# Kernel optimization log

Hardware: AMD Instinct MI355X
Metric: run time of the kernel (lower is better)

The kernel has to match this reference:

```python
import jax, jax.numpy as jnp
import numpy as np

N = 50000
IN_F = 256
HID = 32
HEADS = 4
NEG_SLOPE = 0.2


def _gat_layer(x, edge_index, W, a_src, a_dst, bias):
    # x: [N, Fin]; W: [Fin, H*C]; a_src/a_dst: [H, C]; bias: [H*C]
    n = x.shape[0]
    H, C = a_src.shape
    h = (x @ W).reshape(n, H, C)                     # [N, H, C]
    alpha_src = jnp.einsum('nhc,hc->nh', h, a_src)   # [N, H]
    alpha_dst = jnp.einsum('nhc,hc->nh', h, a_dst)   # [N, H]
    src, dst = edge_index[0], edge_index[1]
    logits = alpha_src[src] + alpha_dst[dst]         # [E, H]
    logits = jax.nn.leaky_relu(logits, negative_slope=NEG_SLOPE)
    # segment softmax over edges grouped by destination node
    seg_max = jax.ops.segment_max(logits, dst, num_segments=n)
    seg_max = jnp.where(jnp.isfinite(seg_max), seg_max, 0.0)
    e = jnp.exp(logits - seg_max[dst])               # [E, H]
    denom = jax.ops.segment_sum(e, dst, num_segments=n)  # [N, H]
    attn = e / (denom[dst] + 1e-16)                  # [E, H]
    msg = h[src] * attn[:, :, None]                  # [E, H, C]
    out = jax.ops.segment_sum(msg, dst, num_segments=n)  # [N, H, C]
    return out.reshape(n, H * C) + bias


def _add_self_loops(edge_index, n):
    # PyG GATConv default add_self_loops=True
    loops = jnp.arange(n, dtype=edge_index.dtype)
    return jnp.concatenate([edge_index, jnp.stack([loops, loops])], axis=1)


def setup_inputs() -> dict:
    key = jax.random.key(0)
    ks = jax.random.split(key, 10)
    x = jax.random.normal(ks[0], (N, IN_F), dtype=jnp.float32)
    edge_index = jax.random.randint(ks[1], (2, 800000), 0, N, dtype=jnp.int64)
    d1 = HEADS * HID
    s1 = 1.0 / np.sqrt(IN_F)
    W1 = jax.random.normal(ks[2], (IN_F, d1), dtype=jnp.float32) * s1
    a_src1 = jax.random.normal(ks[3], (HEADS, HID), dtype=jnp.float32) * 0.1
    a_dst1 = jax.random.normal(ks[4], (HEADS, HID), dtype=jnp.float32) * 0.1
    b1 = jnp.zeros((d1,), dtype=jnp.float32)
    s2 = 1.0 / np.sqrt(d1)
    W2 = jax.random.normal(ks[5], (d1, d1), dtype=jnp.float32) * s2
    a_src2 = jax.random.normal(ks[6], (HEADS, HID), dtype=jnp.float32) * 0.1
    a_dst2 = jax.random.normal(ks[7], (HEADS, HID), dtype=jnp.float32) * 0.1
    b2 = jnp.zeros((d1,), dtype=jnp.float32)
    return {"x": x, "edge_index": edge_index, "W1": W1, "a_src1": a_src1,
            "a_dst1": a_dst1, "b1": b1, "W2": W2, "a_src2": a_src2,
            "a_dst2": a_dst2, "b2": b2}


def reference(x, edge_index, W1, a_src1, a_dst1, b1, W2, a_src2, a_dst2, b2):
    # Inference mode: dropout layers are identity.
    ei = _add_self_loops(edge_index, x.shape[0])
    h = _gat_layer(x, ei, W1, a_src1, a_dst1, b1)
    h = jax.nn.elu(h)
    h = _gat_layer(h, ei, W2, a_src2, a_dst2, b2)
    return h
```

## Files before the change

### kernel.cpp

```cpp
#include <hip/hip_runtime.h>
#include <hip/hip_fp16.h>
#include <math.h>

#define HEADS 4
#define HID 32
#define D1 128
#define IN_FEAT 256
#define NEG_SLOPE 0.2f
#define CAP 64
#define AGG_NODES 4
#define NPASS 8
#define EPT 8

#define WTS_STRIDE_H 72
#define HTS_STRIDE_H 136
#define SMEM_BYTES (128 * 272)

typedef _Float16 half8 __attribute__((ext_vector_type(8)));
typedef float f32x4 __attribute__((ext_vector_type(4)));
typedef long long ll2 __attribute__((ext_vector_type(2)));

static inline int ceil_div(int a, int b) { return (a + b - 1) / b; }

static __device__ inline float2 unpack_h2(unsigned int v) {
    __half2 h = __builtin_bit_cast(__half2, v);
    return __half22float2(h);
}

static __device__ inline void fma_mix_lo(float& a, unsigned int h2, float w) {
    asm("v_fma_mix_f32 %0, %1, %2, %0 op_sel:[0,0,0] op_sel_hi:[1,0,0]"
        : "+v"(a) : "v"(h2), "v"(w));
}
static __device__ inline void fma_mix_hi(float& a, unsigned int h2, float w) {
    asm("v_fma_mix_f32 %0, %1, %2, %0 op_sel:[1,0,0] op_sel_hi:[1,0,0]"
        : "+v"(a) : "v"(h2), "v"(w));
}

__global__ void init_prep(const unsigned int* __restrict__ raw, int* __restrict__ flag,
                          const float* __restrict__ W1, _Float16* __restrict__ WT1,
                          const float* __restrict__ W2, _Float16* __restrict__ WT2) {
    int i = blockIdx.x * blockDim.x + threadIdx.x;
    if (i < IN_FEAT * D1) {
        int k = i >> 7, n = i & 127;
        WT1[(size_t)n * IN_FEAT + k] = (_Float16)W1[i];
    }
    if (i < D1 * D1) {
        int k = i >> 7, n = i & 127;
        WT2[(size_t)n * D1 + k] = (_Float16)W2[i];
    }
    if (blockIdx.x == 0 && threadIdx.x < 64) {
        unsigned int hi = raw[2 * threadIdx.x + 1];
        unsigned long long b = __ballot(hi != 0u);
        if (threadIdx.x == 0) *flag = (b == 0ULL) ? 1 : 0;
    }
}

__device__ void scatter_body(int sbid, const void* __restrict__ raw,
                             const int* __restrict__ flag,
                             int* __restrict__ cnt,
                             unsigned short* __restrict__ slots,
                             int E, int N) {
    const int e0 = (sbid * 256 + (int)threadIdx.x) * EPT;
    const bool wide = (*flag != 0);
    int s[EPT], d[EPT];
    bool val[EPT];
    if (e0 + EPT <= E) {
        if (wide) {
            const ll2* ps = (const ll2*)((const long long*)raw + e0);
            const ll2* pd = (const ll2*)((const long long*)raw + E + e0);
#pragma unroll
            for (int i = 0; i < EPT / 2; ++i) {
                ll2 a = ps[i], b = pd[i];
                s[2 * i] = (int)a[0]; s[2 * i + 1] = (int)a[1];
                d[2 * i] = (int)b[0]; d[2 * i + 1] = (int)b[1];
            }
        } else {
            const int4* ps = (const int4*)((const int*)raw + e0);
            const int4* pd = (const int4*)((const int*)raw + E + e0);
#pragma unroll
            for (int i = 0; i < EPT / 4; ++i) {
                int4 a = ps[i], b = pd[i];
                s[4 * i] = a.x; s[4 * i + 1] = a.y; s[4 * i + 2] = a.z; s[4 * i + 3] = a.w;
                d[4 * i] = b.x; d[4 * i + 1] = b.y; d[4 * i + 2] = b.z; d[4 * i + 3] = b.w;
            }
        }
#pragma unroll
        for (int i = 0; i < EPT; ++i) val[i] = true;
    } else {
#pragma unroll
        for (int i = 0; i < EPT; ++i) {
            int e = e0 + i;
            val[i] = (e < E);
            if (val[i]) {
                if (wide) { s[i] = (int)((const long long*)raw)[e]; d[i] = (int)((const long long*)raw)[E + e]; }
                else      { s[i] = ((const int*)raw)[e];            d[i] = ((const int*)raw)[E + e]; }
            } else { s[i] = 0; d[i] = 0; }
        }
    }

    const int range = (N + NPASS - 1) / NPASS;
    int lo = 0;
    for (int p = 0; p < NPASS; ++p, lo += range) {
        const int hi = lo + range;
#pragma unroll
        for (int i = 0; i < EPT; ++i) {
            if (val[i] && d[i] >= lo && d[i] < hi) {
                int pos = atomicAdd(&cnt[d[i]], 1);
                if (pos < CAP) slots[(size_t)d[i] * CAP + pos] = (unsigned short)s[i];
            }
        }
        __syncthreads();
    }
}

template <int AF16>
__device__ void gemm_body(char* smem, int bid, const void* __restrict__ Ain,
                          const _Float16* __restrict__ WT,
                          _Float16* __restrict__ Hout,
                          const float* __restrict__ a_src,
                          const float* __restrict__ a_dst,
                          float* __restrict__ asrc_out,
                          float* __restrict__ adst_out,
                          int M, int K) {
    const int tid = threadIdx.x;
    const int wave = tid >> 6, lane = tid & 63;
    const int quad = lane >> 4, l16 = lane & 15;
    const int row0 = bid * 128;
    const int m0 = min(row0 + wave * 32 + l16, M - 1);
    const int m1 = min(row0 + wave * 32 + 16 + l16, M - 1);
    const float*    Af = (const float*)Ain;
    const _Float16* Ah = (const _Float16*)Ain;
    const uint4* WTg = (const uint4*)WT;
    const int K8 = K >> 3;

    f32x4 acc[2][8];
#pragma unroll
    for (int r = 0; r < 2; ++r)
#pragma unroll
        for (int c = 0; c < 8; ++c) acc[r][c] = (f32x4){0.f, 0.f, 0.f, 0.f};

    for (int kb = 0; kb < K; kb += 64) {
        __syncthreads();
#pragma unroll
        for (int i = 0; i < 4; ++i) {
            int c = tid + i * 256;
            int n = c >> 3, j = c & 7;
            uint4 v = WTg[(size_t)n * K8 + (kb >> 3) + j];
            *(uint4*)(smem + n * 144 + j * 16) = v;
        }
        __syncthreads();
#pragma unroll
        for (int kc = 0; kc < 2; ++kc) {
            int k0 = kb + kc * 32 + quad * 8;
            half8 a0f, a1f;
            if (AF16) {
                a0f = *(const half8*)(Ah + (size_t)m0 * K + k0);
                a1f = *(const half8*)(Ah + (size_t)m1 * K + k0);
            } else {
                float4 x0 = *(const float4*)(Af + (size_t)m0 * K + k0);
                float4 x1 = *(const float4*)(Af + (size_t)m0 * K + k0 + 4);
                float4 y0 = *(const float4*)(Af + (size_t)m1 * K + k0);
                float4 y1 = *(const float4*)(Af + (size_t)m1 * K + k0 + 4);
                a0f[0] = (_Float16)x0.x; a0f[1] = (_Float16)x0.y;
                a0f[2] = (_Float16)x0.z; a0f[3] = (_Float16)x0.w;
                a0f[4] = (_Float16)x1.x; a0f[5] = (_Float16)x1.y;
                a0f[6] = (_Float16)x1.z; a0f[7] = (_Float16)x1.w;
                a1f[0] = (_Float16)y0.x; a1f[1] = (_Float16)y0.y;
                a1f[2] = (_Float16)y0.z; a1f[3] = (_Float16)y0.w;
                a1f[4] = (_Float16)y1.x; a1f[5] = (_Float16)y1.y;
                a1f[6] = (_Float16)y1.z; a1f[7] = (_Float16)y1.w;
            }
#pragma unroll
            for (int c = 0; c < 8; ++c) {
                half8 bf = *(const half8*)(smem + (c * 16 + l16) * 144 + kc * 64 + quad * 16);
                acc[0][c] = __builtin_amdgcn_mfma_f32_16x16x32_f16(a0f, bf, acc[0][c], 0, 0, 0);
                acc[1][c] = __builtin_amdgcn_mfma_f32_16x16x32_f16(a1f, bf, acc[1][c], 0, 0, 0);
            }
        }
    }

    __syncthreads();
    _Float16* hts = (_Float16*)smem;
#pragma unroll
    for (int r = 0; r < 2; ++r)
#pragma unroll
        for (int c = 0; c < 8; ++c)
#pragma unroll
            for (int g = 0; g < 4; ++g) {
                int row = wave * 32 + r * 16 + quad * 4 + g;
                hts[row * HTS_STRIDE_H + c * 16 + l16] = (_Float16)acc[r][c][g];
            }
    __syncthreads();

    const int r = tid >> 1;
    const int part = tid & 1;
    const int grow = row0 + r;
    const uint4* hrow = (const uint4*)(smem + r * 272 + part * 128);
    if (grow < M) {
        uint4* dv = (uint4*)(Hout + (size_t)grow * 128 + part * 64);
#pragma unroll
        for (int i = 0; i < 8; ++i) dv[i] = hrow[i];
    }
#pragma unroll
    for (int t = 0; t < 2; ++t) {
        int hh = part * 2 + t;
        const uint4* hv = (const uint4*)(smem + r * 272 + hh * 64);
        const float4* as4 = (const float4*)(a_src + hh * HID);
        const float4* ad4 = (const float4*)(a_dst + hh * HID);
        float ps = 0.f, pd = 0.f;
#pragma unroll
        for (int b = 0; b < 4; ++b) {
            uint4 u = hv[b];
            float2 f0 = unpack_h2(u.x), f1 = unpack_h2(u.y);
            float2 f2 = unpack_h2(u.z), f3 = unpack_h2(u.w);
            float4 s0 = as4[b * 2], s1 = as4[b * 2 + 1];
            float4 d0 = ad4[b * 2], d1 = ad4[b * 2 + 1];
            ps += f0.x * s0.x + f0.y * s0.y + f1.x * s0.z + f1.y * s0.w
                + f2.x * s1.x + f2.y * s1.y + f3.x * s1.z + f3.y * s1.w;
            pd += f0.x * d0.x + f0.y * d0.y + f1.x * d0.z + f1.y * d0.w
                + f2.x * d1.x + f2.y * d1.y + f3.x * d1.z + f3.y * d1.w;
        }
        if (grow < M) {
            asrc_out[grow * 4 + hh] = ps;
            adst_out[grow * 4 + hh] = pd;
        }
    }
}

template <int AF16>
__global__ __launch_bounds__(256) void gemm128(const void* __restrict__ Ain,
                                               const _Float16* __restrict__ WT,
                                               _Float16* __restrict__ Hout,
                                               const float* __restrict__ a_src,
                                               const float* __restrict__ a_dst,
                                               float* __restrict__ asrc_out,
                                               float* __restrict__ adst_out,
                                               int M, int K) {
    __shared__ __align__(16) char smem[SMEM_BYTES];
    gemm_body<AF16>(smem, blockIdx.x, Ain, WT, Hout, a_src, a_dst,
                    asrc_out, adst_out, M, K);
}

template <int AF16>
__global__ __launch_bounds__(256) void gemm128_scatter(const void* __restrict__ Ain,
                                                       const _Float16* __restrict__ WT,
                                                       _Float16* __restrict__ Hout,
                                                       const float* __restrict__ a_src,
                                                       const float* __restrict__ a_dst,
                                                       float* __restrict__ asrc_out,
                                                       float* __restrict__ adst_out,
                                                       int M, int K,
                                                       const void* __restrict__ raw,
                                                       const int* __restrict__ flag,
                                                       int* __restrict__ cnt,
                                                       unsigned short* __restrict__ slots,
                                                       int E, int Sg) {
    __shared__ __align__(16) char smem[SMEM_BYTES];
    if ((int)blockIdx.x < Sg) {
        scatter_body(blockIdx.x, raw, flag, cnt, slots, E, M);
        return;
    }
    gemm_body<AF16>(smem, blockIdx.x - Sg, Ain, WT, Hout, a_src, a_dst,
                    asrc_out, adst_out, M, K);
}

__global__ __launch_bounds__(256) void aggregate(const _Float16* __restrict__ hb,
                                                 const int* __restrict__ cnt,
                                                 const unsigned short* __restrict__ slots,
                                                 const float* __restrict__ asrc,
                                                 const float* __restrict__ adst,
                                                 const float* __restrict__ bias,
                                                 float* __restrict__ out32,
                                                 _Float16* __restrict__ out16,
                                                 int N, int apply_elu) {
    const int w = threadIdx.x >> 6;
    const int lane = threadIdx.x & 63;
    const int node = blockIdx.x * AGG_NODES + w;
    const bool live = (node < N);

    __shared__ float wsh[AGG_NODES][CAP][4];
    __shared__ int ssh[AGG_NODES][CAP];

    int cntE = 0, count = 1;
    if (live) {
        cntE = min(cnt[node], CAP - 1);
        count = cntE + 1;
    }
    const unsigned short* nslots = slots + (size_t)node * CAP;

    float4 ad4 = live ? *(const float4*)&adst[node * 4] : make_float4(0.f, 0.f, 0.f, 0.f);

    float lv[4] = {-1e30f, -1e30f, -1e30f, -1e30f};
    if (live && lane < count) {
        int src = (lane < cntE) ? (int)nslots[lane] : node;
        ssh[w][lane] = src << 8;
        float4 as4 = *(const float4*)&asrc[src * 4];
        float t0 = as4.x + ad4.x, t1 = as4.y + ad4.y;
        float t2 = as4.z + ad4.z, t3 = as4.w + ad4.w;
        lv[0] = t0 > 0.f ? t0 : NEG_SLOPE * t0;
        lv[1] = t1 > 0.f ? t1 : NEG_SLOPE * t1;
        lv[2] = t2 > 0.f ? t2 : NEG_SLOPE * t2;
        lv[3] = t3 > 0.f ? t3 : NEG_SLOPE * t3;
    }
    float m[4] = {lv[0], lv[1], lv[2], lv[3]};
#pragma unroll
    for (int off = 32; off >= 1; off >>= 1)
#pragma unroll
        for (int h = 0; h < 4; ++h)
            m[h] = fmaxf(m[h], __shfl_xor(m[h], off, 64));
    float ex[4], sum[4];
#pragma unroll
    for (int h = 0; h < 4; ++h) {
        ex[h] = (lane < count) ? __expf(lv[h] - m[h]) : 0.f;
        sum[h] = ex[h];
    }
#pragma unroll
    for (int off = 32; off >= 1; off >>= 1)
#pragma unroll
        for (int h = 0; h < 4; ++h)
            sum[h] += __shfl_xor(sum[h], off, 64);
    if (live && lane < count) {
        float4 w4;
        w4.x = ex[0] / (sum[0] + 1e-16f);
        w4.y = ex[1] / (sum[1] + 1e-16f);
        w4.z = ex[2] / (sum[2] + 1e-16f);
        w4.w = ex[3] / (sum[3] + 1e-16f);
        *(float4*)&wsh[w][lane][0] = w4;
    }
    __syncthreads();

    const int quarter = lane >> 4;
    const int sub = lane & 15;
    const int hh = sub >> 2;
    const char* hbase = (const char*)hb;
    const int sub16 = sub * 16;

    float acc[8];
#pragma unroll
    for (int i = 0; i < 8; ++i) acc[i] = 0.f;

#define ROW_FMA(u, wt)                                   \
    do {                                                 \
        fma_mix_lo(acc[0], (u).x, (wt));                 \
        fma_mix_hi(acc[1], (u).x, (wt));                 \
        fma_mix_lo(acc[2], (u).y, (wt));                 \
        fma_mix_hi(acc[3], (u).y, (wt));                 \
        fma_mix_lo(acc[4], (u).z, (wt));                 \
        fma_mix_hi(acc[5], (u).z, (wt));                 \
        fma_mix_lo(acc[6], (u).w, (wt));                 \
        fma_mix_hi(acc[7], (u).w, (wt));                 \
    } while (0)

    if (live) {
        int j = quarter;
        if (j + 4 < count) {
            int o0 = ssh[w][j], o1 = ssh[w][j + 4];
            float w0 = wsh[w][j][hh], w1 = wsh[w][j + 4][hh];
            uint4 u0 = *(const uint4*)(hbase + (unsigned)(o0 + sub16));
            uint4 u1 = *(const uint4*)(hbase + (unsigned)(o1 + sub16));
            for (j += 8; j + 4 < count; j += 8) {
                int t0 = ssh[w][j], t1 = ssh[w][j + 4];
                float x0 = wsh[w][j][hh], x1 = wsh[w][j + 4][hh];
                uint4 v0 = *(const uint4*)(hbase + (unsigned)(t0 + sub16));
                uint4 v1 = *(const uint4*)(hbase + (unsigned)(t1 + sub16));
                ROW_FMA(u0, w0);
                ROW_FMA(u1, w1);
                u0 = v0; u1 = v1; w0 = x0; w1 = x1;
            }
            ROW_FMA(u0, w0);
            ROW_FMA(u1, w1);
        }
        if (j < count) {
            int o0 = ssh[w][j];
            float w0 = wsh[w][j][hh];
            uint4 u0 = *(const uint4*)(hbase + (unsigned)(o0 + sub16));
            ROW_FMA(u0, w0);
        }
    }
#undef ROW_FMA

#pragma unroll
    for (int i = 0; i < 8; ++i) {
        acc[i] += __shfl_xor(acc[i], 16, 64);
        acc[i] += __shfl_xor(acc[i], 32, 64);
    }

    if (live && quarter == 0) {
        int ch8 = sub * 8;
        float o[8];
#pragma unroll
        for (int i = 0; i < 8; ++i) o[i] = acc[i] + bias[ch8 + i];
        if (apply_elu) {
#pragma unroll
            for (int i = 0; i < 8; ++i) o[i] = o[i] > 0.f ? o[i] : __expf(o[i]) - 1.f;
        }
        if (out16) {
            __align__(16) _Float16 t[8];
#pragma unroll
            for (int i = 0; i < 8; ++i) t[i] = (_Float16)o[i];
            *(uint4*)&out16[(size_t)node * D1 + ch8] = *(const uint4*)t;
        } else {
            *(float4*)&out32[(size_t)node * D1 + ch8]     = make_float4(o[0], o[1], o[2], o[3]);
            *(float4*)&out32[(size_t)node * D1 + ch8 + 4] = make_float4(o[4], o[5], o[6], o[7]);
        }
    }
}

extern "C" void kernel_launch(void* const* d_in, const int* in_sizes, int n_in,
                              void* d_out, int out_size, void* d_ws, size_t ws_size,
                              hipStream_t stream) {
    const float* x      = (const float*)d_in[0];
    const void*  e_raw  = d_in[1];
    const float* W1     = (const float*)d_in[2];
    const float* a_src1 = (const float*)d_in[3];
    const float* a_dst1 = (const float*)d_in[4];
    const float* b1     = (const float*)d_in[5];
    const float* W2     = (const float*)d_in[6];
    const float* a_src2 = (const float*)d_in[7];
    const float* a_dst2 = (const float*)d_in[8];
    const float* b2     = (const float*)d_in[9];

    const int N  = in_sizes[0] / IN_FEAT;
    const int E  = in_sizes[1] / 2;
    float* out = (float*)d_out;

    char* ws = (char*)d_ws;
    size_t woff = 0;
    auto walloc = [&](size_t bytes) -> char* {
        char* p = ws + woff;
        woff = (woff + bytes + 255) & ~(size_t)255;
        return p;
    };
    int*   flag  = (int*)walloc(4);
    int*   cnt   = (int*)walloc((size_t)N * 4);
    unsigned short* slots = (unsigned short*)walloc((size_t)N * CAP * 2);
    float* asrc  = (float*)walloc((size_t)N * HEADS * 4);
    float* adst  = (float*)walloc((size_t)N * HEADS * 4);
    _Float16* hb  = (_Float16*)walloc((size_t)N * D1 * 2);
    _Float16* o16 = (_Float16*)walloc((size_t)N * D1 * 2);
    _Float16* WT1 = (_Float16*)walloc((size_t)IN_FEAT * D1 * 2);
    _Float16* WT2 = (_Float16*)walloc((size_t)D1 * D1 * 2);

    const int Gg = ceil_div(N, 128);
    const int Sg = ceil_div(E, 256 * EPT);
    const int Ga = ceil_div(N, AGG_NODES);

    hipMemsetAsync(cnt, 0, (size_t)N * 4, stream);
    init_prep<<<ceil_div(IN_FEAT * D1, 256), 256, 0, stream>>>(
        (const unsigned int*)e_raw, flag, W1, WT1, W2, WT2);
    gemm128_scatter<0><<<Sg + Gg, 256, 0, stream>>>(
        x, WT1, hb, a_src1, a_dst1, asrc, adst, N, IN_FEAT,
        e_raw, flag, cnt, slots, E, Sg);
    aggregate<<<Ga, 256, 0, stream>>>(hb, cnt, slots, asrc, adst, b1, nullptr, o16, N, 1);
    gemm128<1><<<Gg, 256, 0, stream>>>(o16, WT2, hb, a_src2, a_dst2, asrc, adst, N, D1);
    aggregate<<<Ga, 256, 0, stream>>>(hb, cnt, slots, asrc, adst, b2, out, nullptr, N, 0);
}
```

Before: 260.5 us.

## Partition scatter blocks by destination range and use half-wave per node aggregation

Each scatter block is now assigned one of eight destination ranges and loops over all edge chunks for that range. This replaces the old scheme where every block walked all eight passes with barriers, and keeps atomics for a given range within one group of blocks. The aggregate kernel maps each node to a half-wave (32 lanes, 8 nodes per block), handling up to 64 neighbors with two slots per lane, which needs fewer cross-lane reductions. The cnt memset is folded into init_prep, removing one launch. The trade-off is that every scatter block re-reads a larger share of the edge list, and each half-wave has fewer lanes in flight for the gather loads.

```diff
diff --git a/kernel.cpp b/kernel.cpp
--- a/kernel.cpp
+++ b/kernel.cpp
@@ -8,8 +8,7 @@
 #define IN_FEAT 256
 #define NEG_SLOPE 0.2f
 #define CAP 64
-#define AGG_NODES 4
-#define NPASS 8
+#define AGG_NODES 8
 #define EPT 8
 
 #define WTS_STRIDE_H 72
@@ -38,8 +37,10 @@
 
 __global__ void init_prep(const unsigned int* __restrict__ raw, int* __restrict__ flag,
                           const float* __restrict__ W1, _Float16* __restrict__ WT1,
-                          const float* __restrict__ W2, _Float16* __restrict__ WT2) {
+                          const float* __restrict__ W2, _Float16* __restrict__ WT2,
+                          int* __restrict__ cnt, int N) {
     int i = blockIdx.x * blockDim.x + threadIdx.x;
+    if (i < N) cnt[i] = 0;
     if (i < IN_FEAT * D1) {
         int k = i >> 7, n = i & 127;
         WT1[(size_t)n * IN_FEAT + k] = (_Float16)W1[i];
@@ -59,49 +60,53 @@
                              const int* __restrict__ flag,
                              int* __restrict__ cnt,
                              unsigned short* __restrict__ slots,
-                             int E, int N) {
-    const int e0 = (sbid * 256 + (int)threadIdx.x) * EPT;
+                             int E, int N, int Sg) {
+    const int grp  = sbid & 7;
+    const int rank = sbid >> 3;
+    const int nrank = (Sg - grp + 7) >> 3;
+    const int range = (N + 7) >> 3;
+    const int lo = grp * range;
+    const int hi = min(lo + range, N);
     const bool wide = (*flag != 0);
-    int s[EPT], d[EPT];
-    bool val[EPT];
-    if (e0 + EPT <= E) {
-        if (wide) {
-            const ll2* ps = (const ll2*)((const long long*)raw + e0);
-            const ll2* pd = (const ll2*)((const long long*)raw + E + e0);
-#pragma unroll
-            for (int i = 0; i < EPT / 2; ++i) {
-                ll2 a = ps[i], b = pd[i];
-                s[2 * i] = (int)a[0]; s[2 * i + 1] = (int)a[1];
-                d[2 * i] = (int)b[0]; d[2 * i + 1] = (int)b[1];
-            }
+    const int NC = (E + 2047) >> 11;
+
+    for (int c = rank; c < NC; c += nrank) {
+        const int e0 = (c << 11) + (int)threadIdx.x * EPT;
+        int s[EPT], d[EPT];
+        bool val[EPT];
+        if (e0 + EPT <= E) {
+            if (wide) {
+                const ll2* ps = (const ll2*)((const long long*)raw + e0);
+                const ll2* pd = (const ll2*)((const long long*)raw + E + e0);
+#pragma unroll
+                for (int i = 0; i < EPT / 2; ++i) {
+                    ll2 a = ps[i], b = pd[i];
+                    s[2 * i] = (int)a[0]; s[2 * i + 1] = (int)a[1];
+                    d[2 * i] = (int)b[0]; d[2 * i + 1] = (int)b[1];
+                }
+            } else {
+                const int4* ps = (const int4*)((const int*)raw + e0);
+                const int4* pd = (const int4*)((const int*)raw + E + e0);
+#pragma unroll
+                for (int i = 0; i < EPT / 4; ++i) {
+                    int4 a = ps[i], b = pd[i];
+                    s[4 * i] = a.x; s[4 * i + 1] = a.y; s[4 * i + 2] = a.z; s[4 * i + 3] = a.w;
+                    d[4 * i] = b.x; d[4 * i + 1] = b.y; d[4 * i + 2] = b.z; d[4 * i + 3] = b.w;
+                }
+            }
+#pragma unroll
+            for (int i = 0; i < EPT; ++i) val[i] = true;
         } else {
-            const int4* ps = (const int4*)((const int*)raw + e0);
-            const int4* pd = (const int4*)((const int*)raw + E + e0);
-#pragma unroll
-            for (int i = 0; i < EPT / 4; ++i) {
-                int4 a = ps[i], b = pd[i];
-                s[4 * i] = a.x; s[4 * i + 1] = a.y; s[4 * i + 2] = a.z; s[4 * i + 3] = a.w;
-                d[4 * i] = b.x; d[4 * i + 1] = b.y; d[4 * i + 2] = b.z; d[4 * i + 3] = b.w;
-            }
-        }
-#pragma unroll
-        for (int i = 0; i < EPT; ++i) val[i] = true;
-    } else {
-#pragma unroll
-        for (int i = 0; i < EPT; ++i) {
-            int e = e0 + i;
-            val[i] = (e < E);
-            if (val[i]) {
-                if (wide) { s[i] = (int)((const long long*)raw)[e]; d[i] = (int)((const long long*)raw)[E + e]; }
-                else      { s[i] = ((const int*)raw)[e];            d[i] = ((const int*)raw)[E + e]; }
-            } else { s[i] = 0; d[i] = 0; }
-        }
-    }
-
-    const int range = (N + NPASS - 1) / NPASS;
-    int lo = 0;
-    for (int p = 0; p < NPASS; ++p, lo += range) {
-        const int hi = lo + range;
+#pragma unroll
+            for (int i = 0; i < EPT; ++i) {
+                int e = e0 + i;
+                val[i] = (e < E);
+                if (val[i]) {
+                    if (wide) { s[i] = (int)((const long long*)raw)[e]; d[i] = (int)((const long long*)raw)[E + e]; }
+                    else      { s[i] = ((const int*)raw)[e];            d[i] = ((const int*)raw)[E + e]; }
+                } else { s[i] = 0; d[i] = -1; }
+            }
+        }
 #pragma unroll
         for (int i = 0; i < EPT; ++i) {
             if (val[i] && d[i] >= lo && d[i] < hi) {
@@ -109,7 +114,6 @@
                 if (pos < CAP) slots[(size_t)d[i] * CAP + pos] = (unsigned short)s[i];
             }
         }
-        __syncthreads();
     }
 }
 
@@ -257,7 +261,7 @@
                                                        int E, int Sg) {
     __shared__ __align__(16) char smem[SMEM_BYTES];
     if ((int)blockIdx.x < Sg) {
-        scatter_body(blockIdx.x, raw, flag, cnt, slots, E, M);
+        scatter_body(blockIdx.x, raw, flag, cnt, slots, E, M, Sg);
         return;
     }
     gemm_body<AF16>(smem, blockIdx.x - Sg, Ain, WT, Hout, a_src, a_dst,
@@ -275,7 +279,10 @@
                                                  int N, int apply_elu) {
     const int w = threadIdx.x >> 6;
     const int lane = threadIdx.x & 63;
-    const int node = blockIdx.x * AGG_NODES + w;
+    const int half = lane >> 5;
+    const int hl = lane & 31;
+    const int idx = w * 2 + half;
+    const int node = blockIdx.x * AGG_NODES + idx;
     const bool live = (node < N);
 
     __shared__ float wsh[AGG_NODES][CAP][4];
@@ -290,47 +297,76 @@
 
     float4 ad4 = live ? *(const float4*)&adst[node * 4] : make_float4(0.f, 0.f, 0.f, 0.f);
 
-    float lv[4] = {-1e30f, -1e30f, -1e30f, -1e30f};
-    if (live && lane < count) {
-        int src = (lane < cntE) ? (int)nslots[lane] : node;
-        ssh[w][lane] = src << 8;
+    const bool v0 = live && (hl < count);
+    const bool v1 = live && (hl + 32 < count);
+    float lv0[4] = {-1e30f, -1e30f, -1e30f, -1e30f};
+    float lv1[4] = {-1e30f, -1e30f, -1e30f, -1e30f};
+    if (v0) {
+        int src = (hl < cntE) ? (int)nslots[hl] : node;
+        ssh[idx][hl] = src << 8;
         float4 as4 = *(const float4*)&asrc[src * 4];
         float t0 = as4.x + ad4.x, t1 = as4.y + ad4.y;
         float t2 = as4.z + ad4.z, t3 = as4.w + ad4.w;
-        lv[0] = t0 > 0.f ? t0 : NEG_SLOPE * t0;
-        lv[1] = t1 > 0.f ? t1 : NEG_SLOPE * t1;
-        lv[2] = t2 > 0.f ? t2 : NEG_SLOPE * t2;
-        lv[3] = t3 > 0.f ? t3 : NEG_SLOPE * t3;
-    }
-    float m[4] = {lv[0], lv[1], lv[2], lv[3]};
-#pragma unroll
-    for (int off = 32; off >= 1; off >>= 1)
+        lv0[0] = t0 > 0.f ? t0 : NEG_SLOPE * t0;
+        lv0[1] = t1 > 0.f ? t1 : NEG_SLOPE * t1;
+        lv0[2] = t2 > 0.f ? t2 : NEG_SLOPE * t2;
+        lv0[3] = t3 > 0.f ? t3 : NEG_SLOPE * t3;
+    }
+    if (v1) {
+        int j = hl + 32;
+        int src = (j < cntE) ? (int)nslots[j] : node;
+        ssh[idx][j] = src << 8;
+        float4 as4 = *(const float4*)&asrc[src * 4];
+        float t0 = as4.x + ad4.x, t1 = as4.y + ad4.y;
+        float t2 = as4.z + ad4.z, t3 = as4.w + ad4.w;
+        lv1[0] = t0 > 0.f ? t0 : NEG_SLOPE * t0;
+        lv1[1] = t1 > 0.f ? t1 : NEG_SLOPE * t1;
+        lv1[2] = t2 > 0.f ? t2 : NEG_SLOPE * t2;
+        lv1[3] = t3 > 0.f ? t3 : NEG_SLOPE * t3;
+    }
+
+    float m[4];
+#pragma unroll
+    for (int h = 0; h < 4; ++h) m[h] = fmaxf(lv0[h], lv1[h]);
+#pragma unroll
+    for (int off = 16; off >= 1; off >>= 1)
 #pragma unroll
         for (int h = 0; h < 4; ++h)
             m[h] = fmaxf(m[h], __shfl_xor(m[h], off, 64));
-    float ex[4], sum[4];
+
+    float e0[4], e1[4], sum[4];
 #pragma unroll
     for (int h = 0; h < 4; ++h) {
-        ex[h] = (lane < count) ? __expf(lv[h] - m[h]) : 0.f;
-        sum[h] = ex[h];
-    }
-#pragma unroll
-    for (int off = 32; off >= 1; off >>= 1)
+        e0[h] = v0 ? __expf(lv0[h] - m[h]) : 0.f;
+        e1[h] = v1 ? __expf(lv1[h] - m[h]) : 0.f;
+        sum[h] = e0[h] + e1[h];
+    }
+#pragma unroll
+    for (int off = 16; off >= 1; off >>= 1)
 #pragma unroll
         for (int h = 0; h < 4; ++h)
             sum[h] += __shfl_xor(sum[h], off, 64);
-    if (live && lane < count) {
+
+    if (v0) {
         float4 w4;
-        w4.x = ex[0] / (sum[0] + 1e-16f);
-        w4.y = ex[1] / (sum[1] + 1e-16f);
-        w4.z = ex[2] / (sum[2] + 1e-16f);
-        w4.w = ex[3] / (sum[3] + 1e-16f);
-        *(float4*)&wsh[w][lane][0] = w4;
+        w4.x = e0[0] / (sum[0] + 1e-16f);
+        w4.y = e0[1] / (sum[1] + 1e-16f);
+        w4.z = e0[2] / (sum[2] + 1e-16f);
+        w4.w = e0[3] / (sum[3] + 1e-16f);
+        *(float4*)&wsh[idx][hl][0] = w4;
+    }
+    if (v1) {
+        float4 w4;
+        w4.x = e1[0] / (sum[0] + 1e-16f);
+        w4.y = e1[1] / (sum[1] + 1e-16f);
+        w4.z = e1[2] / (sum[2] + 1e-16f);
+        w4.w = e1[3] / (sum[3] + 1e-16f);
+        *(float4*)&wsh[idx][hl + 32][0] = w4;
     }
     __syncthreads();
 
-    const int quarter = lane >> 4;
-    const int sub = lane & 15;
+    const int q = hl >> 4;
+    const int sub = hl & 15;
     const int hh = sub >> 2;
     const char* hbase = (const char*)hb;
     const int sub16 = sub * 16;
@@ -352,27 +388,27 @@
     } while (0)
 
     if (live) {
-        int j = quarter;
-        if (j + 4 < count) {
-            int o0 = ssh[w][j], o1 = ssh[w][j + 4];
-            float w0 = wsh[w][j][hh], w1 = wsh[w][j + 4][hh];
+        int j = q;
+        if (j + 2 < count) {
+            int o0 = ssh[idx][j], o1 = ssh[idx][j + 2];
+            float w0 = wsh[idx][j][hh], w1 = wsh[idx][j + 2][hh];
             uint4 u0 = *(const uint4*)(hbase + (unsigned)(o0 + sub16));
             uint4 u1 = *(const uint4*)(hbase + (unsigned)(o1 + sub16));
-            for (j += 8; j + 4 < count; j += 8) {
-                int t0 = ssh[w][j], t1 = ssh[w][j + 4];
-                float x0 = wsh[w][j][hh], x1 = wsh[w][j + 4][hh];
-                uint4 v0 = *(const uint4*)(hbase + (unsigned)(t0 + sub16));
-                uint4 v1 = *(const uint4*)(hbase + (unsigned)(t1 + sub16));
+            for (j += 4; j + 2 < count; j += 4) {
+                int t0 = ssh[idx][j], t1 = ssh[idx][j + 2];
+                float x0 = wsh[idx][j][hh], x1 = wsh[idx][j + 2][hh];
+                uint4 n0 = *(const uint4*)(hbase + (unsigned)(t0 + sub16));
+                uint4 n1 = *(const uint4*)(hbase + (unsigned)(t1 + sub16));
                 ROW_FMA(u0, w0);
                 ROW_FMA(u1, w1);
-                u0 = v0; u1 = v1; w0 = x0; w1 = x1;
+                u0 = n0; u1 = n1; w0 = x0; w1 = x1;
             }
             ROW_FMA(u0, w0);
             ROW_FMA(u1, w1);
         }
         if (j < count) {
-            int o0 = ssh[w][j];
-            float w0 = wsh[w][j][hh];
+            int o0 = ssh[idx][j];
+            float w0 = wsh[idx][j][hh];
             uint4 u0 = *(const uint4*)(hbase + (unsigned)(o0 + sub16));
             ROW_FMA(u0, w0);
         }
@@ -380,12 +416,9 @@
 #undef ROW_FMA
 
 #pragma unroll
-    for (int i = 0; i < 8; ++i) {
-        acc[i] += __shfl_xor(acc[i], 16, 64);
-        acc[i] += __shfl_xor(acc[i], 32, 64);
-    }
-
-    if (live && quarter == 0) {
+    for (int i = 0; i < 8; ++i) acc[i] += __shfl_xor(acc[i], 16, 64);
+
+    if (live && q == 0) {
         int ch8 = sub * 8;
         float o[8];
 #pragma unroll
@@ -444,10 +477,10 @@
     const int Gg = ceil_div(N, 128);
     const int Sg = ceil_div(E, 256 * EPT);
     const int Ga = ceil_div(N, AGG_NODES);
-
-    hipMemsetAsync(cnt, 0, (size_t)N * 4, stream);
-    init_prep<<<ceil_div(IN_FEAT * D1, 256), 256, 0, stream>>>(
-        (const unsigned int*)e_raw, flag, W1, WT1, W2, WT2);
+    const int initN = (N > IN_FEAT * D1) ? N : IN_FEAT * D1;
+
+    init_prep<<<ceil_div(initN, 256), 256, 0, stream>>>(
+        (const unsigned int*)e_raw, flag, W1, WT1, W2, WT2, cnt, N);
     gemm128_scatter<0><<<Sg + Gg, 256, 0, stream>>>(
         x, WT1, hb, a_src1, a_dst1, asrc, adst, N, IN_FEAT,
         e_raw, flag, cnt, slots, E, Sg);
```

Result: faster. 253.1 us (-2.8%).
